# Kernel tuning notes

Hardware: AMD Instinct MI355X
Metric: run time of the kernel (lower is better)

The kernel has to match this reference:

```python
import jax, jax.numpy as jnp
import numpy as np
import math

NUM_HEADS = 16
N_WIRES = 8  # == d_k


def setup_inputs() -> dict:
    key = jax.random.key(0)
    k1, k2, k3, k4 = jax.random.split(key, 4)
    B, S, E = 4, 2048, NUM_HEADS * N_WIRES
    x = jax.random.normal(k1, (B, S, E), dtype=jnp.float32)
    theta = jax.random.normal(k2, (N_WIRES,), dtype=jnp.float32)
    W_combine = jax.random.normal(k3, (E, E), dtype=jnp.float32) * (1.0 / math.sqrt(E))
    b_combine = jax.random.normal(k4, (E,), dtype=jnp.float32) * 0.01
    return {"x": x, "theta": theta, "W_combine": W_combine, "b_combine": b_combine}


def _quantum_heads(x, theta, H, dk):
    # since single-qubit RX gates compose and the state stays a product state.
    B, S, E = x.shape
    proj = x.reshape(B, S, H, dk)  # [B,S,H,dk]
    return jnp.cos(proj + theta)   # theta broadcasts over wires (dk == n_wires)


def reference(x, theta, W_combine, b_combine):
    B, S, E = x.shape
    H, dk = NUM_HEADS, N_WIRES
    qkv = _quantum_heads(x, theta, H, dk)          # [B,S,H,dk]; q = k = v
    qh = jnp.transpose(qkv, (0, 2, 1, 3))           # [B,H,S,dk]
    scores = jnp.einsum('bhqd,bhkd->bhqk', qh, qh) / math.sqrt(dk)
    attn = jax.nn.softmax(scores, axis=-1)          # [B,H,S,S]
    out = jnp.einsum('bhqk,bhkd->bhqd', attn, qh)   # [B,H,S,dk]
    out = jnp.transpose(out, (0, 2, 1, 3)).reshape(B, S, E)
    return out @ W_combine.T + b_combine
```

## Files before the change

### kernel.cpp

```cpp
#include <hip/hip_runtime.h>

typedef _Float16 f16;
typedef _Float16 f16x2 __attribute__((ext_vector_type(2)));
typedef _Float16 f16x4 __attribute__((ext_vector_type(4)));
typedef float    f32x4 __attribute__((ext_vector_type(4)));
typedef unsigned int u32;
typedef unsigned int u32x2v __attribute__((ext_vector_type(2)));

#define NS 2048
#define NH 16
#define NDK 8
#define NE 128
#define CHUNK 512
#define NCHUNK 4
#define CSCALE 0.51006972f

__device__ __forceinline__ float fexp2(float v){
#if __has_builtin(__builtin_amdgcn_exp2f)
  return __builtin_amdgcn_exp2f(v);
#else
  return exp2f(v);
#endif
}

__device__ __forceinline__ f16x2 pkrtz(float a, float b){
  return __builtin_bit_cast(f16x2, __builtin_amdgcn_cvt_pkrtz(a, b));
}

__device__ __forceinline__ float fdot2a(f16x2 a, f16x2 b, float c){
#if __has_builtin(__builtin_amdgcn_fdot2)
  return __builtin_amdgcn_fdot2(a, b, c, false);
#else
  return c + (float)a[0]*(float)b[0] + (float)a[1]*(float)b[1];
#endif
}

__global__ __launch_bounds__(512, 8) void qattn(const float* __restrict__ x,
                                                const float* __restrict__ theta,
                                                float* __restrict__ out){
  __shared__ __align__(16) uint4 Kc[CHUNK];
  __shared__ __align__(16) unsigned short Vc[8*CHUNK];
  __shared__ __align__(16) uint2 Ones[128];

  const int bid  = blockIdx.x;
  const int bh   = bid >> 4;
  const int qc   = bid & 15;
  const int b    = bh >> 4;
  const int h    = bh & 15;
  const int tid  = threadIdx.x;
  const int lane = tid & 63;
  const int w    = tid >> 6;
  const int c    = lane & 15;
  const int grp  = lane >> 4;
  const int g1   = grp & 1;
  const bool lo32 = lane < 32;
  const int dvx  = c & 7;

  const float* xbh = x + (size_t)(b*NS*NH + h)*NDK;

  if(tid < 64){
    uint4 o; o.x = o.y = o.z = o.w = 0x3C003C00u;
    ((uint4*)Ones)[tid] = o;
  }

  const int qrow = qc*128 + w*16 + c;
  const float4 th4 = ((const float4*)theta)[g1];
  const float4 xq = *(const float4*)(xbh + (size_t)qrow*(NH*NDK) + g1*4);
  f16x2 qa = pkrtz(__cosf(xq.x+th4.x)*CSCALE, __cosf(xq.y+th4.y)*CSCALE);
  f16x2 qb = pkrtz(__cosf(xq.z+th4.z)*CSCALE, __cosf(xq.w+th4.w)*CSCALE);
  u32x2v qu = { lo32 ? __builtin_bit_cast(u32, qa) : 0u,
                lo32 ? __builtin_bit_cast(u32, qb) : 0u };
  const f16x4 qf = __builtin_bit_cast(f16x4, qu);

  const uint2* kp  = (const uint2*)Kc + c*2 + g1;
  const uint2* vp0 = (c < 8) ? ((const uint2*)Vc + dvx*128 + ((grp  ) ^ dvx))
                             : Ones;
  const uint2* vp1 = (c < 8) ? ((const uint2*)Vc + dvx*128 + ((4+grp) ^ dvx))
                             : Ones;

  const float4 thA = ((const float4*)theta)[0];
  const float4 thB = ((const float4*)theta)[1];

  const f32x4 z4 = {0.f,0.f,0.f,0.f};
  f32x4 acc0 = z4, acc1 = z4;

  float4 rx0 = *(const float4*)(xbh + (size_t)tid*(NH*NDK));
  float4 rx1 = *(const float4*)(xbh + (size_t)tid*(NH*NDK) + 4);

  for(int cc = 0; cc < NCHUNK; ++cc){
    union { f16 hh[8]; uint4 u; } pk;
    pk.hh[0] = (f16)__cosf(rx0.x + thA.x);
    pk.hh[1] = (f16)__cosf(rx0.y + thA.y);
    pk.hh[2] = (f16)__cosf(rx0.z + thA.z);
    pk.hh[3] = (f16)__cosf(rx0.w + thA.w);
    pk.hh[4] = (f16)__cosf(rx1.x + thB.x);
    pk.hh[5] = (f16)__cosf(rx1.y + thB.y);
    pk.hh[6] = (f16)__cosf(rx1.z + thB.z);
    pk.hh[7] = (f16)__cosf(rx1.w + thB.w);
    Kc[tid] = pk.u;
    {
      int sb = tid >> 2, sl = tid & 3;
      #pragma unroll
      for(int d = 0; d < 8; ++d)
        Vc[d*CHUNK + (((sb ^ d) << 2) | sl)] =
            __builtin_bit_cast(unsigned short, pk.hh[d]);
    }
    __syncthreads();

    if(cc + 1 < NCHUNK){
      const float* nx = xbh + (size_t)((cc+1)*CHUNK + tid)*(NH*NDK);
      rx0 = *(const float4*)(nx);
      rx1 = *(const float4*)(nx + 4);
    }

    #pragma unroll
    for(int m = 0; m < 16; ++m){
      {
        uint2 ka = kp[(2*m+0)*32];
        uint2 va = vp0[m*8];
        f16x4 kf = __builtin_bit_cast(f16x4, ka);
        f16x4 vf = __builtin_bit_cast(f16x4, va);
        f32x4 st = __builtin_amdgcn_mfma_f32_16x16x16f16(kf, qf, z4, 0, 0, 0);
        f16x2 plo = pkrtz(fexp2(st[0]), fexp2(st[1]));
        f16x2 phi = pkrtz(fexp2(st[2]), fexp2(st[3]));
        u32x2v pu = { __builtin_bit_cast(u32, plo), __builtin_bit_cast(u32, phi) };
        f16x4 pf = __builtin_bit_cast(f16x4, pu);
        acc0 = __builtin_amdgcn_mfma_f32_16x16x16f16(vf, pf, acc0, 0, 0, 0);
      }
      {
        uint2 ka = kp[(2*m+1)*32];
        uint2 va = vp1[m*8];
        f16x4 kf = __builtin_bit_cast(f16x4, ka);
        f16x4 vf = __builtin_bit_cast(f16x4, va);
        f32x4 st = __builtin_amdgcn_mfma_f32_16x16x16f16(kf, qf, z4, 0, 0, 0);
        f16x2 plo = pkrtz(fexp2(st[0]), fexp2(st[1]));
        f16x2 phi = pkrtz(fexp2(st[2]), fexp2(st[3]));
        u32x2v pu = { __builtin_bit_cast(u32, plo), __builtin_bit_cast(u32, phi) };
        f16x4 pf = __builtin_bit_cast(f16x4, pu);
        acc1 = __builtin_amdgcn_mfma_f32_16x16x16f16(vf, pf, acc1, 0, 0, 0);
      }
    }

    if(cc + 1 < NCHUNK) __syncthreads();
  }

  f32x4 accT;
  accT[0] = acc0[0]+acc1[0]; accT[1] = acc0[1]+acc1[1];
  accT[2] = acc0[2]+acc1[2]; accT[3] = acc0[3]+acc1[3];
  float den = __shfl(accT[0], 32 + c, 64);
  if(lo32){
    float inv = 1.0f / den;
    float4 o;
    o.x = accT[0]*inv; o.y = accT[1]*inv; o.z = accT[2]*inv; o.w = accT[3]*inv;
    *(float4*)(out + ((size_t)(b*NS + qrow)*NH + h)*NDK + grp*4) = o;
  }
}

__global__ __launch_bounds__(256) void qcomb(const float* __restrict__ W,
                                             const float* __restrict__ bias,
                                             float* __restrict__ io){
  __shared__ __align__(16) u32 Wt[64*132];
  __shared__ __align__(16) u32 A2[32*65];
  const int tid = threadIdx.x;
  const size_t row0 = (size_t)blockIdx.x * 32;

  #pragma unroll
  for(int i=0;i<32;++i){
    int g = tid + 256*i;
    int j = g >> 6, e2 = g & 63;
    const float* wp = W + (size_t)j*NE + 2*e2;
    f16x2 wv = pkrtz(wp[0], wp[1]);
    Wt[e2*132 + j] = __builtin_bit_cast(u32, wv);
  }
  #pragma unroll
  for(int i=0;i<8;++i){
    int g = tid + 256*i;
    int r = g >> 6, e2 = g & 63;
    const float* ap = io + (row0 + r)*NE + 2*e2;
    f16x2 av = pkrtz(ap[0], ap[1]);
    A2[r*65 + e2] = __builtin_bit_cast(u32, av);
  }
  __syncthreads();

  const int tr = tid >> 4, tc = tid & 15;
  float acc0[8] = {0,0,0,0,0,0,0,0};
  float acc1[8] = {0,0,0,0,0,0,0,0};
  for(int e2=0; e2<64; ++e2){
    f16x2 a0 = __builtin_bit_cast(f16x2, A2[tr*65 + e2]);
    f16x2 a1 = __builtin_bit_cast(f16x2, A2[(tr+16)*65 + e2]);
    const u32* wr = &Wt[e2*132 + tc*8];
    #pragma unroll
    for(int cj=0; cj<8; ++cj){
      f16x2 wv = __builtin_bit_cast(f16x2, wr[cj]);
      acc0[cj] = fdot2a(a0, wv, acc0[cj]);
      acc1[cj] = fdot2a(a1, wv, acc1[cj]);
    }
  }

  float4 b0 = *(const float4*)(bias + tc*8);
  float4 b1 = *(const float4*)(bias + tc*8 + 4);
  float* o0 = io + (row0 + tr)*NE + tc*8;
  float* o1 = io + (row0 + tr + 16)*NE + tc*8;
  float4 v;
  v.x = acc0[0]+b0.x; v.y = acc0[1]+b0.y; v.z = acc0[2]+b0.z; v.w = acc0[3]+b0.w;
  *(float4*)(o0) = v;
  v.x = acc0[4]+b1.x; v.y = acc0[5]+b1.y; v.z = acc0[6]+b1.z; v.w = acc0[7]+b1.w;
  *(float4*)(o0+4) = v;
  v.x = acc1[0]+b0.x; v.y = acc1[1]+b0.y; v.z = acc1[2]+b0.z; v.w = acc1[3]+b0.w;
  *(float4*)(o1) = v;
  v.x = acc1[4]+b1.x; v.y = acc1[5]+b1.y; v.z = acc1[6]+b1.z; v.w = acc1[7]+b1.w;
  *(float4*)(o1+4) = v;
}

extern "C" void kernel_launch(void* const* d_in, const int* in_sizes, int n_in,
                              void* d_out, int out_size, void* d_ws, size_t ws_size,
                              hipStream_t stream) {
  (void)in_sizes; (void)n_in; (void)out_size; (void)d_ws; (void)ws_size;
  const float* x     = (const float*)d_in[0];
  const float* theta = (const float*)d_in[1];
  const float* W     = (const float*)d_in[2];
  const float* bias  = (const float*)d_in[3];
  float* out = (float*)d_out;

  qattn<<<1024, 512, 0, stream>>>(x, theta, out);
  qcomb<<<256, 256, 0, stream>>>(W, bias, out);
}
```

Baseline: 49.50 us.

## Precompute cos K/V tiles in a separate kernel and stream them via async LDS loads

Adds a qcos kernel that computes cos(x+theta) once per element in fp16 and writes a K buffer plus a pre-transposed V buffer to workspace. Previously each of the 16 query-chunk blocks per head recomputed these values. The attention kernel now double-buffers K/V chunks into LDS with global_load_lds and issues the prefetch for the next chunk during compute, with one barrier per chunk. Q is read from the fp16 K buffer and scaled there. This adds an extra launch and a workspace round trip, and lowers the occupancy hint from 8 to 4 because of the larger LDS footprint.

```diff
diff --git a/kernel.cpp b/kernel.cpp
--- a/kernel.cpp
+++ b/kernel.cpp
@@ -35,118 +35,139 @@
 #endif
 }
 
-__global__ __launch_bounds__(512, 8) void qattn(const float* __restrict__ x,
-                                                const float* __restrict__ theta,
+#define GLOAD16(g, l) __builtin_amdgcn_global_load_lds( \
+    (const __attribute__((address_space(1))) u32*)(g), \
+    (__attribute__((address_space(3))) u32*)(l), 16, 0, 0)
+
+__global__ __launch_bounds__(256) void qcos(const float* __restrict__ x,
+                                            const float* __restrict__ theta,
+                                            u32* __restrict__ kbuf,
+                                            u32* __restrict__ vbuf){
+  __shared__ __align__(16) uint4 Lt[16*17];
+  const int bid = blockIdx.x;
+  const int b   = bid >> 7;
+  const int t   = bid & 127;
+  const int tid = threadIdx.x;
+
+  const float4 thA = ((const float4*)theta)[0];
+  const float4 thB = ((const float4*)theta)[1];
+
+  {
+    const int sl = tid & 15, h = tid >> 4;
+    const int s  = t*16 + sl;
+    const float* xp = x + ((size_t)(b*NS + s)*NE + h*NDK);
+    const float4 x0 = ((const float4*)xp)[0];
+    const float4 x1 = ((const float4*)xp)[1];
+    union { f16 hh[8]; uint4 u; } pk;
+    pk.hh[0] = (f16)__cosf(x0.x + thA.x);
+    pk.hh[1] = (f16)__cosf(x0.y + thA.y);
+    pk.hh[2] = (f16)__cosf(x0.z + thA.z);
+    pk.hh[3] = (f16)__cosf(x0.w + thA.w);
+    pk.hh[4] = (f16)__cosf(x1.x + thB.x);
+    pk.hh[5] = (f16)__cosf(x1.y + thB.y);
+    pk.hh[6] = (f16)__cosf(x1.z + thB.z);
+    pk.hh[7] = (f16)__cosf(x1.w + thB.w);
+    ((uint4*)kbuf)[(size_t)(b*16 + h)*NS + s] = pk.u;
+    Lt[h*17 + sl] = pk.u;
+  }
+  __syncthreads();
+
+  {
+    const int h  = tid >> 4;
+    const int d  = (tid >> 1) & 7;
+    const int gp = tid & 1;
+    const unsigned short* Ls = (const unsigned short*)Lt;
+    union { unsigned short us[8]; uint4 u; } pk;
+    #pragma unroll
+    for(int j = 0; j < 8; ++j)
+      pk.us[j] = Ls[(h*17 + 8*gp + j)*8 + d];
+    ((uint4*)vbuf)[((size_t)(b*16 + h)*128 + t)*16 + d*2 + gp] = pk.u;
+  }
+}
+
+#define QTILE(T, VPO, KPO, ACC) do{ \
+    uint2 ka_ = (KPO)[(T)*32]; \
+    uint2 va_ = (VPO)[(T)*32]; \
+    f16x4 kf_ = __builtin_bit_cast(f16x4, ka_); \
+    f16x4 vf_ = __builtin_bit_cast(f16x4, va_); \
+    f32x4 st_ = __builtin_amdgcn_mfma_f32_16x16x16f16(kf_, qf, z4, 0, 0, 0); \
+    f16x2 plo_ = pkrtz(fexp2(st_[0]), fexp2(st_[1])); \
+    f16x2 phi_ = pkrtz(fexp2(st_[2]), fexp2(st_[3])); \
+    u32x2v pu_ = { __builtin_bit_cast(u32, plo_), __builtin_bit_cast(u32, phi_) }; \
+    f16x4 pf_ = __builtin_bit_cast(f16x4, pu_); \
+    ACC = __builtin_amdgcn_mfma_f32_16x16x16f16(vf_, pf_, ACC, 0, 0, 0); \
+  }while(0)
+
+__global__ __launch_bounds__(512, 4) void qattn(const u32* __restrict__ kbuf,
+                                                const u32* __restrict__ vbuf,
                                                 float* __restrict__ out){
-  __shared__ __align__(16) uint4 Kc[CHUNK];
-  __shared__ __align__(16) unsigned short Vc[8*CHUNK];
-  __shared__ __align__(16) uint2 Ones[128];
+  __shared__ __align__(16) u32 Kc[2][2048];
+  __shared__ __align__(16) u32 Vt[2][2048];
+  __shared__ __align__(16) u32 OnesR[512];
 
   const int bid  = blockIdx.x;
   const int bh   = bid >> 4;
   const int qc   = bid & 15;
-  const int b    = bh >> 4;
-  const int h    = bh & 15;
   const int tid  = threadIdx.x;
   const int lane = tid & 63;
   const int w    = tid >> 6;
   const int c    = lane & 15;
   const int grp  = lane >> 4;
   const int g1   = grp & 1;
-  const bool lo32 = lane < 32;
-  const int dvx  = c & 7;
-
-  const float* xbh = x + (size_t)(b*NS*NH + h)*NDK;
-
-  if(tid < 64){
-    uint4 o; o.x = o.y = o.z = o.w = 0x3C003C00u;
-    ((uint4*)Ones)[tid] = o;
-  }
+  const bool lo32  = lane < 32;
+  const bool creal = c < 8;
+
+  const u32* kb = kbuf + (size_t)bh*8192;
+  const u32* vb = vbuf + (size_t)bh*8192;
+
+  OnesR[tid] = 0x3C003C00u;
+
+  const u32* gk = kb + (size_t)tid*4;
+  const u32* gv = vb + (size_t)tid*4;
 
   const int qrow = qc*128 + w*16 + c;
-  const float4 th4 = ((const float4*)theta)[g1];
-  const float4 xq = *(const float4*)(xbh + (size_t)qrow*(NH*NDK) + g1*4);
-  f16x2 qa = pkrtz(__cosf(xq.x+th4.x)*CSCALE, __cosf(xq.y+th4.y)*CSCALE);
-  f16x2 qb = pkrtz(__cosf(xq.z+th4.z)*CSCALE, __cosf(xq.w+th4.w)*CSCALE);
-  u32x2v qu = { lo32 ? __builtin_bit_cast(u32, qa) : 0u,
-                lo32 ? __builtin_bit_cast(u32, qb) : 0u };
-  const f16x4 qf = __builtin_bit_cast(f16x4, qu);
-
-  const uint2* kp  = (const uint2*)Kc + c*2 + g1;
-  const uint2* vp0 = (c < 8) ? ((const uint2*)Vc + dvx*128 + ((grp  ) ^ dvx))
-                             : Ones;
-  const uint2* vp1 = (c < 8) ? ((const uint2*)Vc + dvx*128 + ((4+grp) ^ dvx))
-                             : Ones;
-
-  const float4 thA = ((const float4*)theta)[0];
-  const float4 thB = ((const float4*)theta)[1];
-
-  const f32x4 z4 = {0.f,0.f,0.f,0.f};
+  uint2 qv = make_uint2(0u, 0u);
+  if(lo32) qv = *(const uint2*)(kb + (size_t)qrow*4 + g1*2);
+  f16x4 q4 = __builtin_bit_cast(f16x4, qv);
+  q4 *= (f16)CSCALE;
+  const f16x4 qf = q4;
+
+  const u32 vlane = ((u32)(c & 7))*32u + ((u32)grp)*8u;
+  const char* onesc = (const char*)OnesR;
+
+  const f32x4 z4 = {0.f, 0.f, 0.f, 0.f};
   f32x4 acc0 = z4, acc1 = z4;
 
-  float4 rx0 = *(const float4*)(xbh + (size_t)tid*(NH*NDK));
-  float4 rx1 = *(const float4*)(xbh + (size_t)tid*(NH*NDK) + 4);
+  GLOAD16(gk, &Kc[0][w*256]);
+  GLOAD16(gv, &Vt[0][w*256]);
 
   for(int cc = 0; cc < NCHUNK; ++cc){
-    union { f16 hh[8]; uint4 u; } pk;
-    pk.hh[0] = (f16)__cosf(rx0.x + thA.x);
-    pk.hh[1] = (f16)__cosf(rx0.y + thA.y);
-    pk.hh[2] = (f16)__cosf(rx0.z + thA.z);
-    pk.hh[3] = (f16)__cosf(rx0.w + thA.w);
-    pk.hh[4] = (f16)__cosf(rx1.x + thB.x);
-    pk.hh[5] = (f16)__cosf(rx1.y + thB.y);
-    pk.hh[6] = (f16)__cosf(rx1.z + thB.z);
-    pk.hh[7] = (f16)__cosf(rx1.w + thB.w);
-    Kc[tid] = pk.u;
-    {
-      int sb = tid >> 2, sl = tid & 3;
-      #pragma unroll
-      for(int d = 0; d < 8; ++d)
-        Vc[d*CHUNK + (((sb ^ d) << 2) | sl)] =
-            __builtin_bit_cast(unsigned short, pk.hh[d]);
+    __syncthreads();
+    if(cc + 1 < NCHUNK){
+      GLOAD16(gk + (size_t)(cc+1)*2048, &Kc[(cc+1)&1][w*256]);
+      GLOAD16(gv + (size_t)(cc+1)*2048, &Vt[(cc+1)&1][w*256]);
     }
-    __syncthreads();
-
-    if(cc + 1 < NCHUNK){
-      const float* nx = xbh + (size_t)((cc+1)*CHUNK + tid)*(NH*NDK);
-      rx0 = *(const float4*)(nx);
-      rx1 = *(const float4*)(nx + 4);
+    const uint2* kp = (const uint2*)&Kc[cc&1][0] + c*2 + g1;
+    const char*  vc = (const char*)&Vt[cc&1][0] + vlane;
+    #pragma unroll
+    for(int o = 0; o < 4; ++o){
+      const uint2* kpo = kp + o*256;
+      const uint2* vpo = (const uint2*)(creal ? vc + o*2048 : onesc);
+      QTILE(0, vpo, kpo, acc0);
+      QTILE(1, vpo, kpo, acc1);
+      QTILE(2, vpo, kpo, acc0);
+      QTILE(3, vpo, kpo, acc1);
+      QTILE(4, vpo, kpo, acc0);
+      QTILE(5, vpo, kpo, acc1);
+      QTILE(6, vpo, kpo, acc0);
+      QTILE(7, vpo, kpo, acc1);
     }
-
-    #pragma unroll
-    for(int m = 0; m < 16; ++m){
-      {
-        uint2 ka = kp[(2*m+0)*32];
-        uint2 va = vp0[m*8];
-        f16x4 kf = __builtin_bit_cast(f16x4, ka);
-        f16x4 vf = __builtin_bit_cast(f16x4, va);
-        f32x4 st = __builtin_amdgcn_mfma_f32_16x16x16f16(kf, qf, z4, 0, 0, 0);
-        f16x2 plo = pkrtz(fexp2(st[0]), fexp2(st[1]));
-        f16x2 phi = pkrtz(fexp2(st[2]), fexp2(st[3]));
-        u32x2v pu = { __builtin_bit_cast(u32, plo), __builtin_bit_cast(u32, phi) };
-        f16x4 pf = __builtin_bit_cast(f16x4, pu);
-        acc0 = __builtin_amdgcn_mfma_f32_16x16x16f16(vf, pf, acc0, 0, 0, 0);
-      }
-      {
-        uint2 ka = kp[(2*m+1)*32];
-        uint2 va = vp1[m*8];
-        f16x4 kf = __builtin_bit_cast(f16x4, ka);
-        f16x4 vf = __builtin_bit_cast(f16x4, va);
-        f32x4 st = __builtin_amdgcn_mfma_f32_16x16x16f16(kf, qf, z4, 0, 0, 0);
-        f16x2 plo = pkrtz(fexp2(st[0]), fexp2(st[1]));
-        f16x2 phi = pkrtz(fexp2(st[2]), fexp2(st[3]));
-        u32x2v pu = { __builtin_bit_cast(u32, plo), __builtin_bit_cast(u32, phi) };
-        f16x4 pf = __builtin_bit_cast(f16x4, pu);
-        acc1 = __builtin_amdgcn_mfma_f32_16x16x16f16(vf, pf, acc1, 0, 0, 0);
-      }
-    }
-
-    if(cc + 1 < NCHUNK) __syncthreads();
   }
 
   f32x4 accT;
   accT[0] = acc0[0]+acc1[0]; accT[1] = acc0[1]+acc1[1];
   accT[2] = acc0[2]+acc1[2]; accT[3] = acc0[3]+acc1[3];
+  const int b = bh >> 4, h = bh & 15;
   float den = __shfl(accT[0], 32 + c, 64);
   if(lo32){
     float inv = 1.0f / den;
@@ -215,13 +236,16 @@
 extern "C" void kernel_launch(void* const* d_in, const int* in_sizes, int n_in,
                               void* d_out, int out_size, void* d_ws, size_t ws_size,
                               hipStream_t stream) {
-  (void)in_sizes; (void)n_in; (void)out_size; (void)d_ws; (void)ws_size;
+  (void)in_sizes; (void)n_in; (void)out_size; (void)ws_size;
   const float* x     = (const float*)d_in[0];
   const float* theta = (const float*)d_in[1];
   const float* W     = (const float*)d_in[2];
   const float* bias  = (const float*)d_in[3];
   float* out = (float*)d_out;
-
-  qattn<<<1024, 512, 0, stream>>>(x, theta, out);
+  u32* kbuf = (u32*)d_ws;
+  u32* vbuf = kbuf + 524288;
+
+  qcos <<<512, 256, 0, stream>>>(x, theta, kbuf, vbuf);
+  qattn<<<1024, 512, 0, stream>>>(kbuf, vbuf, out);
   qcomb<<<256, 256, 0, stream>>>(W, bias, out);
 }
```

Result: slower. 53.70 us (+8.5%).
